# Performance work log

Hardware: AMD Instinct MI355X
Metric: run time of the kernel (lower is better)

Reference implementation:

```python
import jax, jax.numpy as jnp
import numpy as np
from jax import lax

B, IMG = 2, 512
FMC, HID, A, NC = 1024, 512, 9, 21
RED, POOL, TOP, IOU_THR = 16, 7, 20, 0.3
NEG = -1e30
# 3 scales x 3 aspect ratios (w, h)
ANCHOR_WH = np.array([[s * np.sqrt(r), s / np.sqrt(r)] for s in (64.0, 128.0, 256.0) for r in (0.5, 1.0, 2.0)], dtype=np.float32)


def conv(x, w, b, stride, pad):
    y = lax.conv_general_dilated(x, w, (stride, stride), pad, dimension_numbers=('NCHW', 'OIHW', 'NCHW'))
    return y + b[None, :, None, None]


def make_anchors(H, W, stride):
    cy = (jnp.arange(H, dtype=jnp.float32) + 0.5) * stride
    cx = (jnp.arange(W, dtype=jnp.float32) + 0.5) * stride
    cyg, cxg = jnp.meshgrid(cy, cx, indexing='ij')  # [H,W]
    wh = jnp.asarray(ANCHOR_WH)  # [A,2]
    w2 = wh[None, None, :, 0] / 2
    h2 = wh[None, None, :, 1] / 2
    cxg = cxg[:, :, None]
    cyg = cyg[:, :, None]
    boxes = jnp.stack([cxg - w2, cyg - h2, cxg + w2, cyg + h2], axis=-1)  # [H,W,A,4]
    return boxes.reshape(-1, 4)


def box_iou(b, boxes):
    # b [4], boxes [N,4], (x1,y1,x2,y2)
    ix1 = jnp.maximum(b[0], boxes[:, 0])
    iy1 = jnp.maximum(b[1], boxes[:, 1])
    ix2 = jnp.minimum(b[2], boxes[:, 2])
    iy2 = jnp.minimum(b[3], boxes[:, 3])
    inter = jnp.maximum(ix2 - ix1, 0.0) * jnp.maximum(iy2 - iy1, 0.0)
    ab = jnp.maximum(b[2] - b[0], 0.0) * jnp.maximum(b[3] - b[1], 0.0)
    ar = jnp.maximum(boxes[:, 2] - boxes[:, 0], 0.0) * jnp.maximum(boxes[:, 3] - boxes[:, 1], 0.0)
    return inter / (ab + ar - inter + 1e-8)


def nms_one(boxes, scores):
    # greedy NMS, fixed TOP selections
    n = scores.shape[0]
    idxs = jnp.arange(n)

    def step(s, _):
        i = jnp.argmax(s)
        b, sc = boxes[i], s[i]
        s = jnp.where((box_iou(b, boxes) > IOU_THR) | (idxs == i), NEG, s)
        return s, (b, sc)

    _, (bs, ss) = lax.scan(step, scores, None, length=TOP)
    return bs, ss  # [TOP,4], [TOP]


def roi_align_one(fm_b, boxes):
    # fm_b [C,H,W], boxes [R,4] in image coords -> [R,C,POOL,POOL]
    C, H, W = fm_b.shape
    b = boxes / RED
    t = (jnp.arange(POOL, dtype=jnp.float32) + 0.5) / POOL
    xs = b[:, 0:1] + jnp.maximum(b[:, 2] - b[:, 0], 0.0)[:, None] * t[None]  # [R,P]
    ys = b[:, 1:2] + jnp.maximum(b[:, 3] - b[:, 1], 0.0)[:, None] * t[None]
    x = jnp.clip(xs[:, None, :], 0.0, W - 1.0) * jnp.ones((1, POOL, 1), jnp.float32)  # [R,P,P]
    y = jnp.clip(ys[:, :, None], 0.0, H - 1.0) * jnp.ones((1, 1, POOL), jnp.float32)
    x0f, y0f = jnp.floor(x), jnp.floor(y)
    x0, y0 = x0f.astype(jnp.int32), y0f.astype(jnp.int32)
    x1 = jnp.minimum(x0 + 1, W - 1)
    y1 = jnp.minimum(y0 + 1, H - 1)
    lx, ly = x - x0f, y - y0f
    v00 = fm_b[:, y0, x0]
    v01 = fm_b[:, y0, x1]
    v10 = fm_b[:, y1, x0]
    v11 = fm_b[:, y1, x1]  # [C,R,P,P]
    out = v00 * (1 - ly) * (1 - lx) + v01 * (1 - ly) * lx + v10 * ly * (1 - lx) + v11 * ly * lx
    return out.transpose(1, 0, 2, 3)


def setup_inputs() -> dict:
    key = jax.random.key(0)
    ks = jax.random.split(key, 16)
    s = 0.02
    return {
        'img': jax.random.normal(ks[0], (B, 3, IMG, IMG), jnp.float32),
        'img_id': jnp.arange(B, dtype=jnp.int32),
        'cnn_w': jax.random.normal(ks[1], (FMC, 3, RED, RED), jnp.float32) * s,
        'cnn_b': jnp.zeros((FMC,), jnp.float32),
        'rpn_w': jax.random.normal(ks[2], (HID, FMC, 3, 3), jnp.float32) * s,
        'rpn_b': jnp.zeros((HID,), jnp.float32),
        'rpn_reg_w': jax.random.normal(ks[3], (A * 4, HID, 1, 1), jnp.float32) * s,
        'rpn_reg_b': jnp.zeros((A * 4,), jnp.float32),
        'rpn_cls_w': jax.random.normal(ks[4], (A, HID, 1, 1), jnp.float32) * s,
        'rpn_cls_b': jnp.zeros((A,), jnp.float32),
        'fc_w': jax.random.normal(ks[5], (FMC * POOL * POOL, 1024), jnp.float32) * 0.005,
        'fc_b': jnp.zeros((1024,), jnp.float32),
        'reg_w': jax.random.normal(ks[6], (1024, 4), jnp.float32) * s,
        'reg_b': jnp.zeros((4,), jnp.float32),
        'cls_w': jax.random.normal(ks[7], (1024, NC), jnp.float32) * s,
        'cls_b': jnp.zeros((NC,), jnp.float32),
    }


def reference(img, img_id, cnn_w, cnn_b, rpn_w, rpn_b, rpn_reg_w, rpn_reg_b, rpn_cls_w, rpn_cls_b, fc_w, fc_b, reg_w, reg_b, cls_w, cls_b):
    fm = jax.nn.relu(conv(img, cnn_w, cnn_b, RED, 'VALID'))  # [B,1024,32,32]
    Bn, C, H, W = fm.shape
    # sliding-window(3x3, stride 1) + per-slice RPN == 3x3 SAME conv + 1x1 heads
    h = jax.nn.relu(conv(fm, rpn_w, rpn_b, 1, 'SAME'))
    rpn_reg = conv(h, rpn_reg_w, rpn_reg_b, 1, 'SAME').transpose(0, 2, 3, 1).reshape(Bn, -1, 4)  # (h,w,a) order
    rpn_cls = conv(h, rpn_cls_w, rpn_cls_b, 1, 'SAME').transpose(0, 2, 3, 1).reshape(Bn, -1)
    anchors = make_anchors(H, W, RED)  # [H*W*A,4]
    nms_reg, nms_cls = jax.vmap(nms_one)(rpn_reg + anchors[None], rpn_cls)  # [B,TOP,4],[B,TOP]
    pooled = jax.vmap(roi_align_one)(fm[img_id], nms_reg)  # [B,TOP,C,P,P]
    flat = pooled.reshape(Bn * TOP, -1)
    hf = jax.nn.relu(flat @ fc_w + fc_b)
    rcnn_reg = (hf @ reg_w + reg_b).reshape(Bn, -1, 4)
    rcnn_cls = (hf @ cls_w + cls_b).reshape(Bn, TOP, -1)
    return rpn_reg, rpn_cls, nms_reg, nms_cls, rcnn_reg, rcnn_cls, anchors
```

## Files before the change

### kernel.cpp

```cpp
#include <hip/hip_runtime.h>
#include <math.h>


#define NEGV (-1e30f)

typedef unsigned short u16;
typedef float v4f __attribute__((ext_vector_type(4)));
typedef short short8 __attribute__((ext_vector_type(8)));

#define O_RPN_REG 0
#define O_RPN_CLS 73728
#define O_NMS_REG 92160
#define O_NMS_CLS 92320
#define O_RCNN_REG 92360
#define O_RCNN_CLS 92520
#define O_ANCH 93360

#define W_FM   0u
#define W_ZERO 2097152u
#define W_PROP 3145728u
#define W_SCR  3219456u
#define W_FLAT 3237888u
#define W_HF   5244928u
#define W_A1H  5285888u
#define W_A1L  6072320u
#define W_B1H  6858752u
#define W_B1L  7251968u
#define W_FMH  7645184u
#define W_FML  8693760u
#define W_B2H  9742336u
#define W_B2L  12101632u
#define W_PART 14460928u

static __device__ __forceinline__ float relu_(float v) { return fmaxf(v, 0.0f); }

static __device__ __forceinline__ void gload16(const void* g, void* l) {
    __builtin_amdgcn_global_load_lds(
        (const __attribute__((address_space(1))) unsigned int*)g,
        (__attribute__((address_space(3))) unsigned int*)l, 16, 0, 0);
}

static __device__ __forceinline__ u16 bf16_rtne(float x) {
    unsigned int u = __float_as_uint(x);
    unsigned int r = u + 0x7fffu + ((u >> 16) & 1u);
    return (u16)(r >> 16);
}
static __device__ __forceinline__ void split2(float x, u16& h, u16& l) {
    h = bf16_rtne(x);
    const float hf = __uint_as_float(((unsigned int)h) << 16);
    l = bf16_rtne(x - hf);
}
static __device__ __forceinline__ void split8_store(const float* v, u16* dsth, u16* dstl) {
    uint4 H, Lo;
    u16 h0, l0, h1, l1;
    split2(v[0], h0, l0); split2(v[1], h1, l1);
    H.x = (unsigned)h0 | ((unsigned)h1 << 16); Lo.x = (unsigned)l0 | ((unsigned)l1 << 16);
    split2(v[2], h0, l0); split2(v[3], h1, l1);
    H.y = (unsigned)h0 | ((unsigned)h1 << 16); Lo.y = (unsigned)l0 | ((unsigned)l1 << 16);
    split2(v[4], h0, l0); split2(v[5], h1, l1);
    H.z = (unsigned)h0 | ((unsigned)h1 << 16); Lo.z = (unsigned)l0 | ((unsigned)l1 << 16);
    split2(v[6], h0, l0); split2(v[7], h1, l1);
    H.w = (unsigned)h0 | ((unsigned)h1 << 16); Lo.w = (unsigned)l0 | ((unsigned)l1 << 16);
    *(uint4*)dsth = H; *(uint4*)dstl = Lo;
}

static __device__ __forceinline__ void anchor_wh(int a, float& w2, float& h2) {
    double s = (a < 3) ? 64.0 : (a < 6) ? 128.0 : 256.0;
    int rm = a - (a / 3) * 3;
    double r = (rm == 0) ? 0.5 : (rm == 1) ? 1.0 : 2.0;
    double sq = sqrt(r);
    w2 = (float)(s * sq) * 0.5f;
    h2 = (float)(s / sq) * 0.5f;
}

__global__ void k_prep_a1(const float* __restrict__ img, u16* __restrict__ a1h, u16* __restrict__ a1l,
                          float* __restrict__ zbuf) {
    if (blockIdx.x == 0 && threadIdx.x < 64) zbuf[threadIdx.x] = 0.0f;
    const int idx = blockIdx.x * 256 + threadIdx.x;
    const int m = idx / 192, kq = (idx - m * 192) * 4;
    const int b = m >> 10, i = (m >> 5) & 31, j = m & 31;
    const int c = kq >> 8, rem = kq & 255, y = rem >> 4, x = rem & 15;
    const float4 v = *(const float4*)(img + ((size_t)((b * 3 + c) * 512 + i * 16 + y)) * 512 + j * 16 + x);
    ushort4 H, Lo;
    split2(v.x, H.x, Lo.x); split2(v.y, H.y, Lo.y);
    split2(v.z, H.z, Lo.z); split2(v.w, H.w, Lo.w);
    *(ushort4*)(a1h + (size_t)idx * 4) = H;
    *(ushort4*)(a1l + (size_t)idx * 4) = Lo;
}

__global__ void k_split4(const float* __restrict__ src, u16* __restrict__ h, u16* __restrict__ l, int n4) {
    const int idx = blockIdx.x * 256 + threadIdx.x;
    if (idx >= n4) return;
    const float4 v = *(const float4*)(src + (size_t)idx * 4);
    ushort4 H, Lo;
    split2(v.x, H.x, Lo.x); split2(v.y, H.y, Lo.y);
    split2(v.z, H.z, Lo.z); split2(v.w, H.w, Lo.w);
    *(ushort4*)(h + (size_t)idx * 4) = H;
    *(ushort4*)(l + (size_t)idx * 4) = Lo;
}

__global__ __launch_bounds__(256) void k_prep_w2(const float* __restrict__ w,
        u16* __restrict__ bh, u16* __restrict__ bl) {
    __shared__ __align__(16) u16 sh[9216];
    __shared__ __align__(16) u16 sl[9216];
    const int oc = blockIdx.x;
    const float* p = w + (size_t)oc * 9216;
    for (int i = threadIdx.x * 4; i < 9216; i += 1024) {
        const float4 v = *(const float4*)(p + i);
        ushort4 H, Lo;
        split2(v.x, H.x, Lo.x); split2(v.y, H.y, Lo.y);
        split2(v.z, H.z, Lo.z); split2(v.w, H.w, Lo.w);
        *(ushort4*)(sh + i) = H;
        *(ushort4*)(sl + i) = Lo;
    }
    __syncthreads();
    const int ic4 = threadIdx.x * 4;
#pragma unroll
    for (int d = 0; d < 9; ++d) {
        ushort4 H, Lo;
        H.x = sh[(ic4 + 0) * 9 + d]; Lo.x = sl[(ic4 + 0) * 9 + d];
        H.y = sh[(ic4 + 1) * 9 + d]; Lo.y = sl[(ic4 + 1) * 9 + d];
        H.z = sh[(ic4 + 2) * 9 + d]; Lo.z = sl[(ic4 + 2) * 9 + d];
        H.w = sh[(ic4 + 3) * 9 + d]; Lo.w = sl[(ic4 + 3) * 9 + d];
        const size_t o = (size_t)oc * 9216 + d * 1024 + ic4;
        *(ushort4*)(bh + o) = H;
        *(ushort4*)(bl + o) = Lo;
    }
}

template<int MODE>
__global__ __launch_bounds__(256, 3) void k_gemm(
        const u16* __restrict__ Agh, const u16* __restrict__ Agl,
        const u16* __restrict__ Bgh, const u16* __restrict__ Bgl,
        const float* __restrict__ bias, float* __restrict__ Cout, float* __restrict__ Cout2,
        const int KA, const int KB, const int nchunk, const int ldc, const int do_bias_relu,
        u16* __restrict__ outH, u16* __restrict__ outL, const float* __restrict__ zbuf) {
    __shared__ __align__(16) u16 AsH[2 * 128 * 32];
    __shared__ __align__(16) u16 AsL[2 * 128 * 32];
    __shared__ __align__(16) u16 BsH[2 * 64 * 32];
    __shared__ __align__(16) u16 BsL[2 * 64 * 32];
    const int tid = threadIdx.x;
    const int w = tid >> 6, L = tid & 63;
    const int q = L >> 4, lr = L & 15;
    const int wm = w >> 1, wn = w & 1;
    const int m0 = blockIdx.x * 128, n0 = blockIdx.y * 64;
    const int zbase = blockIdx.z * nchunk;
    float* C;
    if (MODE == 1) {
        C = (blockIdx.z < 4) ? (Cout + (size_t)blockIdx.z * (2048u * 512u))
                             : (Cout2 + (size_t)(blockIdx.z - 4) * (2048u * 512u));
    } else {
        C = (blockIdx.z == 0) ? Cout : Cout2;
    }
    const int seg = L & 3, rsub = L >> 2;

    u16* lseg[6];
    int lsz[6];
    const u16* gbase[6];
    int arow_b[6], arow_i[6], arow_j[6];
    int kindv[6];
#pragma unroll
    for (int s = 0; s < 6; ++s) {
        const int idx = w * 6 + s;
        int kind, inst;
        if (idx < 8)       { kind = 0; inst = idx; }
        else if (idx < 16) { kind = 1; inst = idx - 8; }
        else if (idx < 20) { kind = 2; inst = idx - 16; }
        else               { kind = 3; inst = idx - 20; }
        kindv[s] = kind;
        const int r = inst * 16 + rsub;
        u16* lb = (kind == 0) ? AsH : (kind == 1) ? AsL : (kind == 2) ? BsH : BsL;
        lseg[s] = lb + r * 32 + seg * 8;
        lsz[s] = (kind < 2) ? (128 * 32) : (64 * 32);
        arow_b[s] = 0; arow_i[s] = 0; arow_j[s] = 0;
        if (kind >= 2) {
            const u16* gb = (kind == 2) ? Bgh : Bgl;
            gbase[s] = gb + (size_t)(n0 + r) * KB + seg * 8;
        } else if (MODE == 0) {
            const u16* gb = (kind == 0) ? Agh : Agl;
            gbase[s] = gb + (size_t)(m0 + r) * KA + seg * 8;
        } else {
            const int m = m0 + r;
            arow_b[s] = m >> 10; arow_i[s] = (m >> 5) & 31; arow_j[s] = m & 31;
            gbase[s] = (kind == 0) ? Agh : Agl;
        }
    }

    v4f acc[4][2];
#pragma unroll
    for (int t = 0; t < 4; ++t)
#pragma unroll
        for (int u2 = 0; u2 < 2; ++u2) acc[t][u2] = (v4f){0.f, 0.f, 0.f, 0.f};

#define ISSUE(c_, bb_) do { \
    int d_, ic_, kB_; \
    if (MODE == 0) { const int g_ = zbase + (c_); kB_ = g_ * 32; d_ = 0; ic_ = kB_; } \
    else { const int g_ = zbase + (c_); d_ = g_ >> 5; ic_ = (g_ & 31) << 5; kB_ = d_ * 1024 + ic_; } \
    const int di_ = d_ / 3, dj_ = d_ - di_ * 3; \
    _Pragma("unroll") \
    for (int s = 0; s < 6; ++s) { \
        const u16* gsrc_; \
        if (kindv[s] >= 2) gsrc_ = gbase[s] + kB_; \
        else if (MODE == 0) gsrc_ = gbase[s] + ic_; \
        else { \
            const int y_ = arow_i[s] + di_ - 1, x_ = arow_j[s] + dj_ - 1; \
            const bool ok_ = ((unsigned)y_ < 32u) && ((unsigned)x_ < 32u); \
            const int yc_ = ok_ ? y_ : 0, xc_ = ok_ ? x_ : 0; \
            const u16* ga_ = gbase[s] + (size_t)((arow_b[s] * 32 + yc_) * 32 + xc_) * 1024 + ic_ + seg * 8; \
            gsrc_ = ok_ ? ga_ : (const u16*)zbuf; \
        } \
        gload16(gsrc_, lseg[s] + (bb_) * lsz[s]); \
    } \
} while (0)

    int cur = 0;
    ISSUE(0, 0);
    for (int c = 0; c < nchunk; ++c) {
        __syncthreads();
        if (c + 1 < nchunk) ISSUE(c + 1, cur ^ 1);
        const int ao = cur * (128 * 32), bo = cur * (64 * 32);
        short8 ah[4], al[4], bh[2], bl[2];
#pragma unroll
        for (int t = 0; t < 4; ++t) {
            ah[t] = *(const short8*)(AsH + ao + (wm * 64 + t * 16 + lr) * 32 + q * 8);
            al[t] = *(const short8*)(AsL + ao + (wm * 64 + t * 16 + lr) * 32 + q * 8);
        }
#pragma unroll
        for (int u2 = 0; u2 < 2; ++u2) {
            bh[u2] = *(const short8*)(BsH + bo + (wn * 32 + u2 * 16 + lr) * 32 + q * 8);
            bl[u2] = *(const short8*)(BsL + bo + (wn * 32 + u2 * 16 + lr) * 32 + q * 8);
        }
#pragma unroll
        for (int t = 0; t < 4; ++t)
#pragma unroll
            for (int u2 = 0; u2 < 2; ++u2) {
                acc[t][u2] = __builtin_amdgcn_mfma_f32_16x16x32_bf16(ah[t], bh[u2], acc[t][u2], 0, 0, 0);
                acc[t][u2] = __builtin_amdgcn_mfma_f32_16x16x32_bf16(ah[t], bl[u2], acc[t][u2], 0, 0, 0);
                acc[t][u2] = __builtin_amdgcn_mfma_f32_16x16x32_bf16(al[t], bh[u2], acc[t][u2], 0, 0, 0);
            }
        cur ^= 1;
    }
#undef ISSUE

#pragma unroll
    for (int t = 0; t < 4; ++t) {
        const int row = m0 + wm * 64 + t * 16 + q * 4;
#pragma unroll
        for (int u2 = 0; u2 < 2; ++u2) {
            const int col = n0 + wn * 32 + u2 * 16 + lr;
            const float bv = do_bias_relu ? bias[col] : 0.f;
#pragma unroll
            for (int r = 0; r < 4; ++r) {
                float vv = acc[t][u2][r];
                if (do_bias_relu) vv = relu_(vv + bv);
                C[(size_t)(row + r) * ldc + col] = vv;
                if (MODE == 0 && outH != nullptr) {
                    u16 hh, ll; split2(vv, hh, ll);
                    outH[(size_t)(row + r) * 1024 + col] = hh;
                    outL[(size_t)(row + r) * 1024 + col] = ll;
                }
            }
        }
    }
}

__global__ void k_c1_reduce(const float* __restrict__ p1, const float* __restrict__ cb,
                            float* __restrict__ fm, u16* __restrict__ fmh, u16* __restrict__ fml) {
    const size_t o = ((size_t)blockIdx.x * 256 + threadIdx.x) * 4;
    float4 a = *(const float4*)(fm + o);
    const float4 b4 = *(const float4*)(p1 + o);
    const float4 bb = *(const float4*)(cb + (o & 1023));
    a.x = relu_(a.x + b4.x + bb.x);
    a.y = relu_(a.y + b4.y + bb.y);
    a.z = relu_(a.z + b4.z + bb.z);
    a.w = relu_(a.w + b4.w + bb.w);
    *(float4*)(fm + o) = a;
    ushort4 H, Lo;
    split2(a.x, H.x, Lo.x); split2(a.y, H.y, Lo.y);
    split2(a.z, H.z, Lo.z); split2(a.w, H.w, Lo.w);
    *(ushort4*)(fmh + o) = H;
    *(ushort4*)(fml + o) = Lo;
}

__global__ __launch_bounds__(64) void k_rpn_heads(const float* __restrict__ partA,
        const float* __restrict__ partB,
        const float* __restrict__ rpnb,
        const float* __restrict__ regw, const float* __restrict__ regb,
        const float* __restrict__ clsw, const float* __restrict__ clsb,
        float* __restrict__ out, float* __restrict__ prop, float* __restrict__ scr) {
    __shared__ __align__(16) float hrow[512];
    const int m = blockIdx.x, tid = threadIdx.x;
    const int b = m >> 10, qd = m & 1023, ii = qd >> 5, jj = qd & 31;
    for (int i = tid * 4; i < 512; i += 256) {
        const size_t ro = (size_t)m * 512 + i;
        const float4 a0 = *(const float4*)(partA + ro);
        const float4 a1 = *(const float4*)(partA + 1048576u + ro);
        const float4 a2 = *(const float4*)(partA + 2097152u + ro);
        const float4 a3 = *(const float4*)(partA + 3145728u + ro);
        const float4 a4 = *(const float4*)(partB + ro);
        const float4 a5 = *(const float4*)(partB + 1048576u + ro);
        const float4 bb = *(const float4*)(rpnb + i);
        float4 o;
        o.x = relu_(a0.x + a1.x + a2.x + a3.x + a4.x + a5.x + bb.x);
        o.y = relu_(a0.y + a1.y + a2.y + a3.y + a4.y + a5.y + bb.y);
        o.z = relu_(a0.z + a1.z + a2.z + a3.z + a4.z + a5.z + bb.z);
        o.w = relu_(a0.w + a1.w + a2.w + a3.w + a4.w + a5.w + bb.w);
        *(float4*)&hrow[i] = o;
    }
    __syncthreads();
    if (tid < 45) {
        const int isreg = (tid < 36);
        const float* wp = isreg ? (regw + (size_t)tid * 512) : (clsw + (size_t)(tid - 36) * 512);
        float acc2 = isreg ? regb[tid] : clsb[tid - 36];
        for (int k = 0; k < 512; k += 4) {
            const float4 wv = *(const float4*)(wp + k);
            acc2 += hrow[k + 0] * wv.x; acc2 += hrow[k + 1] * wv.y;
            acc2 += hrow[k + 2] * wv.z; acc2 += hrow[k + 3] * wv.w;
        }
        if (isreg) {
            out[O_RPN_REG + (size_t)b * 36864 + qd * 36 + tid] = acc2;
            const int a = tid >> 2, cc = tid & 3;
            float w2, h2; anchor_wh(a, w2, h2);
            const float cx = ((float)jj + 0.5f) * 16.f, cy = ((float)ii + 0.5f) * 16.f;
            const float av = (cc == 0) ? cx - w2 : (cc == 1) ? cy - h2 : (cc == 2) ? cx + w2 : cy + h2;
            prop[(size_t)b * 36864 + qd * 36 + tid] = acc2 + av;
        } else {
            const int n = tid - 36;
            out[O_RPN_CLS + (size_t)b * 9216 + qd * 9 + n] = acc2;
            scr[(size_t)b * 9216 + qd * 9 + n] = acc2;
        }
    }
    if (b == 0 && tid >= 48 && tid < 57) {
        const int a = tid - 48;
        float w2, h2; anchor_wh(a, w2, h2);
        const float cx = ((float)jj + 0.5f) * 16.f, cy = ((float)ii + 0.5f) * 16.f;
        const float4 av4 = make_float4(cx - w2, cy - h2, cx + w2, cy + h2);
        *(float4*)(out + O_ANCH + (size_t)(qd * 9 + a) * 4) = av4;
    }
}

__global__ __launch_bounds__(512) void k_nms3(const float* __restrict__ prop,
        const float* __restrict__ scr, float* __restrict__ out) {
    __shared__ float wv_[2][8];
    __shared__ int wi_[2][8];
    const int b = blockIdx.x, tid = threadIdx.x;
    const int lane = tid & 63, wid = tid >> 6;
    const float* P = prop + (size_t)b * 36864;
    float4 bx[18]; float sv[18];
#pragma unroll
    for (int k = 0; k < 18; ++k) {
        const int i = tid * 18 + k;
        bx[k] = *(const float4*)(P + (size_t)i * 4);
        sv[k] = scr[b * 9216 + i];
    }
    for (int t = 0; t < 20; ++t) {
        float bv = -3.4e38f; int bi = 0;
#pragma unroll
        for (int k = 0; k < 18; ++k)
            if (sv[k] > bv) { bv = sv[k]; bi = tid * 18 + k; }
#pragma unroll
        for (int off = 1; off < 64; off <<= 1) {
            const float ov = __shfl_xor(bv, off);
            const int oi = __shfl_xor(bi, off);
            if (ov > bv || (ov == bv && oi < bi)) { bv = ov; bi = oi; }
        }
        if (lane == 0) { wv_[t & 1][wid] = bv; wi_[t & 1][wid] = bi; }
        __syncthreads();
        float rb = wv_[t & 1][0]; int sel = wi_[t & 1][0];
#pragma unroll
        for (int j = 1; j < 8; ++j) {
            const float v2 = wv_[t & 1][j]; const int i2 = wi_[t & 1][j];
            if (v2 > rb || (v2 == rb && i2 < sel)) { rb = v2; sel = i2; }
        }
        const float4 bb = *(const float4*)(P + (size_t)sel * 4);
        if (tid == 0) {
            *(float4*)(out + O_NMS_REG + (size_t)(b * 20 + t) * 4) = bb;
            out[O_NMS_CLS + b * 20 + t] = rb;
        }
        const float ab2 = fmaxf(bb.z - bb.x, 0.f) * fmaxf(bb.w - bb.y, 0.f);
#pragma unroll
        for (int k = 0; k < 18; ++k) {
            const float ix1 = fmaxf(bb.x, bx[k].x), iy1 = fmaxf(bb.y, bx[k].y);
            const float ix2 = fminf(bb.z, bx[k].z), iy2 = fminf(bb.w, bx[k].w);
            const float inter = fmaxf(ix2 - ix1, 0.f) * fmaxf(iy2 - iy1, 0.f);
            const float ar2 = fmaxf(bx[k].z - bx[k].x, 0.f) * fmaxf(bx[k].w - bx[k].y, 0.f);
            const float iou = inter / (ab2 + ar2 - inter + 1e-8f);
            if (iou > 0.3f || (tid * 18 + k) == sel) sv[k] = NEGV;
        }
    }
}

__global__ __launch_bounds__(256) void k_roi(const float* __restrict__ fm,
        const int* __restrict__ img_id, const float* __restrict__ nreg,
        float* __restrict__ flat) {
    __shared__ float tile[12544];
    const int c0 = blockIdx.x * 256;
    const int roi = blockIdx.y, b = blockIdx.z;
    const float* bx = nreg + (size_t)(b * 20 + roi) * 4;
    const float b0 = bx[0] * 0.0625f, b1 = bx[1] * 0.0625f;
    const float b2 = bx[2] * 0.0625f, b3 = bx[3] * 0.0625f;
    const float wd = fmaxf(b2 - b0, 0.f), hg = fmaxf(b3 - b1, 0.f);
    const int bb = img_id[b];
    const float* fmb = fm + (size_t)bb * (32 * 32 * 1024);
    const int c = c0 + threadIdx.x;
    for (int py = 0; py < 7; ++py) {
        const float tyv = ((float)py + 0.5f) / 7.0f;
        const float ycv = fminf(fmaxf(b1 + hg * tyv, 0.f), 31.f);
        const float y0f = floorf(ycv);
        const int y0 = (int)y0f, y1 = min(y0 + 1, 31);
        const float ly = ycv - y0f, omly = 1.f - ly;
        for (int px = 0; px < 7; ++px) {
            const float txv = ((float)px + 0.5f) / 7.0f;
            const float xcv = fminf(fmaxf(b0 + wd * txv, 0.f), 31.f);
            const float x0f = floorf(xcv);
            const int x0 = (int)x0f, x1 = min(x0 + 1, 31);
            const float lx = xcv - x0f, omlx = 1.f - lx;
            const int o00 = ((y0 * 32) + x0) << 10, o01 = ((y0 * 32) + x1) << 10;
            const int o10 = ((y1 * 32) + x0) << 10, o11 = ((y1 * 32) + x1) << 10;
            const float v00 = fmb[o00 + c], v01 = fmb[o01 + c];
            const float v10 = fmb[o10 + c], v11 = fmb[o11 + c];
            tile[threadIdx.x * 49 + py * 7 + px] =
                ((v00 * omly) * omlx) + ((v01 * omly) * lx)
                + ((v10 * ly) * omlx) + ((v11 * ly) * lx);
        }
    }
    __syncthreads();
    const size_t ob = (size_t)(b * 20 + roi) * 50176 + (size_t)c0 * 49;
    for (int i = threadIdx.x * 4; i < 12544; i += 1024)
        *(float4*)(flat + ob + i) = *(const float4*)&tile[i];
}

__global__ void k_hf_init(const float* __restrict__ fcb, float* __restrict__ hf) {
    const int i = blockIdx.x * 256 + threadIdx.x;
    if (i < 40 * 1024) hf[i] = fcb[i & 1023];
}

__global__ __launch_bounds__(256, 2) void k_fc_mfma(const float* __restrict__ flat,
        const float* __restrict__ fcw, float* __restrict__ hf) {
    __shared__ __align__(16) u16 AsH[4 * 48 * 8];
    __shared__ __align__(16) u16 AsL[4 * 48 * 8];
    __shared__ __align__(16) u16 BsH[4 * 256 * 8];
    __shared__ __align__(16) u16 BsL[4 * 256 * 8];
    const int tid = threadIdx.x;
    const int w = tid >> 6, L = tid & 63, q = L >> 4, lr = L & 15;
    const int n0 = blockIdx.x * 256, kb = blockIdx.y * 512;
    if (tid < 32) {
        const int oct = tid >> 3, m = 40 + (tid & 7);
        *(uint4*)(AsH + (oct * 48 + m) * 8) = make_uint4(0, 0, 0, 0);
        *(uint4*)(AsL + (oct * 48 + m) * 8) = make_uint4(0, 0, 0, 0);
    }
    const int am = tid >> 2, aoct = tid & 3;
    const float* abase = flat + (size_t)am * 50176 + kb + aoct * 8;
    const float* bcol = fcw + n0 + tid;

    v4f acc[3][4];
#pragma unroll
    for (int mt = 0; mt < 3; ++mt)
#pragma unroll
        for (int nt = 0; nt < 4; ++nt) acc[mt][nt] = (v4f){0.f, 0.f, 0.f, 0.f};

    float areg[8];
    float breg[4][8];

#define LOADF(c_) do { \
    if (tid < 160) { \
        const float4 u_ = *(const float4*)(abase + (c_) * 32); \
        const float4 v_ = *(const float4*)(abase + (c_) * 32 + 4); \
        areg[0] = u_.x; areg[1] = u_.y; areg[2] = u_.z; areg[3] = u_.w; \
        areg[4] = v_.x; areg[5] = v_.y; areg[6] = v_.z; areg[7] = v_.w; \
    } \
    _Pragma("unroll") \
    for (int o_ = 0; o_ < 4; ++o_) \
        _Pragma("unroll") \
        for (int j_ = 0; j_ < 8; ++j_) \
            breg[o_][j_] = bcol[(size_t)(kb + (c_) * 32 + o_ * 8 + j_) * 1024]; \
} while (0)

    LOADF(0);
    for (int c = 0; c < 16; ++c) {
        __syncthreads();
        if (tid < 160)
            split8_store(areg, AsH + (aoct * 48 + am) * 8, AsL + (aoct * 48 + am) * 8);
#pragma unroll
        for (int o = 0; o < 4; ++o)
            split8_store(breg[o], BsH + (o * 256 + tid) * 8, BsL + (o * 256 + tid) * 8);
        __syncthreads();
        if (c + 1 < 16) LOADF(c + 1);
        short8 ah[3], al[3], bh2[4], bl2[4];
#pragma unroll
        for (int mt = 0; mt < 3; ++mt) {
            ah[mt] = *(const short8*)(AsH + (q * 48 + mt * 16 + lr) * 8);
            al[mt] = *(const short8*)(AsL + (q * 48 + mt * 16 + lr) * 8);
        }
#pragma unroll
        for (int nt = 0; nt < 4; ++nt) {
            bh2[nt] = *(const short8*)(BsH + (q * 256 + w * 64 + nt * 16 + lr) * 8);
            bl2[nt] = *(const short8*)(BsL + (q * 256 + w * 64 + nt * 16 + lr) * 8);
        }
#pragma unroll
        for (int mt = 0; mt < 3; ++mt)
#pragma unroll
            for (int nt = 0; nt < 4; ++nt) {
                acc[mt][nt] = __builtin_amdgcn_mfma_f32_16x16x32_bf16(ah[mt], bh2[nt], acc[mt][nt], 0, 0, 0);
                acc[mt][nt] = __builtin_amdgcn_mfma_f32_16x16x32_bf16(ah[mt], bl2[nt], acc[mt][nt], 0, 0, 0);
                acc[mt][nt] = __builtin_amdgcn_mfma_f32_16x16x32_bf16(al[mt], bh2[nt], acc[mt][nt], 0, 0, 0);
            }
    }
#undef LOADF

#pragma unroll
    for (int mt = 0; mt < 3; ++mt) {
#pragma unroll
        for (int nt = 0; nt < 4; ++nt) {
#pragma unroll
            for (int r = 0; r < 4; ++r) {
                const int row = mt * 16 + q * 4 + r;
                if (row < 40)
                    atomicAdd(hf + (size_t)row * 1024 + n0 + w * 64 + nt * 16 + lr, acc[mt][nt][r]);
            }
        }
    }
}

__global__ __launch_bounds__(64) void k_heads(const float* __restrict__ hf,
        const float* __restrict__ regw, const float* __restrict__ regb,
        const float* __restrict__ clsw, const float* __restrict__ clsb,
        float* __restrict__ out) {
    __shared__ __align__(16) float hrow[1024];
    const int m = blockIdx.x, tid = threadIdx.x;
    for (int i = tid * 4; i < 1024; i += 256) {
        const float4 v = *(const float4*)(hf + (size_t)m * 1024 + i);
        hrow[i + 0] = relu_(v.x); hrow[i + 1] = relu_(v.y);
        hrow[i + 2] = relu_(v.z); hrow[i + 3] = relu_(v.w);
    }
    __syncthreads();
    if (tid < 25) {
        float acc2 = 0.f;
        if (tid < 4) {
            for (int k = 0; k < 1024; ++k) acc2 += hrow[k] * regw[(size_t)k * 4 + tid];
            out[O_RCNN_REG + m * 4 + tid] = acc2 + regb[tid];
        } else {
            const int n = tid - 4;
            for (int k = 0; k < 1024; ++k) acc2 += hrow[k] * clsw[(size_t)k * 21 + n];
            out[O_RCNN_CLS + m * 21 + n] = acc2 + clsb[n];
        }
    }
}

extern "C" void kernel_launch(void* const* d_in, const int* in_sizes, int n_in,
                              void* d_out, int out_size, void* d_ws, size_t ws_size,
                              hipStream_t stream) {
    (void)in_sizes; (void)n_in; (void)out_size; (void)ws_size;
    const float* img       = (const float*)d_in[0];
    const int*   img_id    = (const int*)  d_in[1];
    const float* cnn_w     = (const float*)d_in[2];
    const float* cnn_b     = (const float*)d_in[3];
    const float* rpn_w     = (const float*)d_in[4];
    const float* rpn_b     = (const float*)d_in[5];
    const float* rpn_reg_w = (const float*)d_in[6];
    const float* rpn_reg_b = (const float*)d_in[7];
    const float* rpn_cls_w = (const float*)d_in[8];
    const float* rpn_cls_b = (const float*)d_in[9];
    const float* fc_w      = (const float*)d_in[10];
    const float* fc_b      = (const float*)d_in[11];
    const float* reg_w     = (const float*)d_in[12];
    const float* reg_b     = (const float*)d_in[13];
    const float* cls_w     = (const float*)d_in[14];
    const float* cls_b     = (const float*)d_in[15];
    float* out = (float*)d_out;
    float* ws  = (float*)d_ws;

    float* fm   = ws + W_FM;
    float* zbuf = ws + W_ZERO;
    float* prop = ws + W_PROP;
    float* scr  = ws + W_SCR;
    float* flat = ws + W_FLAT;
    float* hf   = ws + W_HF;
    u16* a1h = (u16*)(ws + W_A1H);
    u16* a1l = (u16*)(ws + W_A1L);
    u16* b1h = (u16*)(ws + W_B1H);
    u16* b1l = (u16*)(ws + W_B1L);
    u16* fmh = (u16*)(ws + W_FMH);
    u16* fml = (u16*)(ws + W_FML);
    u16* b2h = (u16*)(ws + W_B2H);
    u16* b2l = (u16*)(ws + W_B2L);
    float* partA = ws + W_FLAT;
    float* partB = ws + W_PART;

    k_prep_a1<<<1536, 256, 0, stream>>>(img, a1h, a1l, zbuf);
    k_split4<<<768, 256, 0, stream>>>(cnn_w, b1h, b1l, 196608);
    k_prep_w2<<<512, 256, 0, stream>>>(rpn_w, b2h, b2l);
    k_gemm<0><<<dim3(16, 16, 2), 256, 0, stream>>>(a1h, a1l, b1h, b1l, cnn_b, fm, partB,
                                                   768, 768, 12, 1024, 0, nullptr, nullptr, zbuf);
    k_c1_reduce<<<2048, 256, 0, stream>>>(partB, cnn_b, fm, fmh, fml);
    k_gemm<1><<<dim3(16, 8, 6), 256, 0, stream>>>(fmh, fml, b2h, b2l, nullptr, partA, partB,
                                                  1024, 9216, 48, 512, 0, nullptr, nullptr, zbuf);
    k_rpn_heads<<<2048, 64, 0, stream>>>(partA, partB, rpn_b, rpn_reg_w, rpn_reg_b, rpn_cls_w, rpn_cls_b,
                                         out, prop, scr);
    k_nms3<<<2, 512, 0, stream>>>(prop, scr, out);
    k_roi<<<dim3(4, 20, 2), 256, 0, stream>>>(fm, img_id, out + O_NMS_REG, flat);
    k_hf_init<<<160, 256, 0, stream>>>(fc_b, hf);
    k_fc_mfma<<<dim3(4, 98), 256, 0, stream>>>(flat, fc_w, hf);
    k_heads<<<40, 64, 0, stream>>>(hf, reg_w, reg_b, cls_w, cls_b, out);
}
```

Measured before the change: 593.2 us.

## Merge prep kernels, batch RPN head rows, fold hf init, narrow FC tiles

New measurement: 605.4 us. 2.1% more time.

```diff
diff --git a/kernel.cpp b/kernel.cpp
--- a/kernel.cpp
+++ b/kernel.cpp
@@ -73,58 +73,58 @@
     h2 = (float)(s / sq) * 0.5f;
 }
 
-__global__ void k_prep_a1(const float* __restrict__ img, u16* __restrict__ a1h, u16* __restrict__ a1l,
-                          float* __restrict__ zbuf) {
-    if (blockIdx.x == 0 && threadIdx.x < 64) zbuf[threadIdx.x] = 0.0f;
-    const int idx = blockIdx.x * 256 + threadIdx.x;
-    const int m = idx / 192, kq = (idx - m * 192) * 4;
-    const int b = m >> 10, i = (m >> 5) & 31, j = m & 31;
-    const int c = kq >> 8, rem = kq & 255, y = rem >> 4, x = rem & 15;
-    const float4 v = *(const float4*)(img + ((size_t)((b * 3 + c) * 512 + i * 16 + y)) * 512 + j * 16 + x);
-    ushort4 H, Lo;
-    split2(v.x, H.x, Lo.x); split2(v.y, H.y, Lo.y);
-    split2(v.z, H.z, Lo.z); split2(v.w, H.w, Lo.w);
-    *(ushort4*)(a1h + (size_t)idx * 4) = H;
-    *(ushort4*)(a1l + (size_t)idx * 4) = Lo;
-}
-
-__global__ void k_split4(const float* __restrict__ src, u16* __restrict__ h, u16* __restrict__ l, int n4) {
-    const int idx = blockIdx.x * 256 + threadIdx.x;
-    if (idx >= n4) return;
-    const float4 v = *(const float4*)(src + (size_t)idx * 4);
-    ushort4 H, Lo;
-    split2(v.x, H.x, Lo.x); split2(v.y, H.y, Lo.y);
-    split2(v.z, H.z, Lo.z); split2(v.w, H.w, Lo.w);
-    *(ushort4*)(h + (size_t)idx * 4) = H;
-    *(ushort4*)(l + (size_t)idx * 4) = Lo;
-}
-
-__global__ __launch_bounds__(256) void k_prep_w2(const float* __restrict__ w,
-        u16* __restrict__ bh, u16* __restrict__ bl) {
+__global__ __launch_bounds__(256) void k_prep_all(
+        const float* __restrict__ img, u16* __restrict__ a1h, u16* __restrict__ a1l,
+        float* __restrict__ zbuf,
+        const float* __restrict__ cnnw, u16* __restrict__ b1h, u16* __restrict__ b1l,
+        const float* __restrict__ rpnw, u16* __restrict__ b2h, u16* __restrict__ b2l) {
     __shared__ __align__(16) u16 sh[9216];
     __shared__ __align__(16) u16 sl[9216];
-    const int oc = blockIdx.x;
-    const float* p = w + (size_t)oc * 9216;
-    for (int i = threadIdx.x * 4; i < 9216; i += 1024) {
-        const float4 v = *(const float4*)(p + i);
+    const int bx = blockIdx.x, tid = threadIdx.x;
+    if (bx < 1536) {
+        if (bx == 0 && tid < 64) zbuf[tid] = 0.0f;
+        const int idx = bx * 256 + tid;
+        const int m = idx / 192, kq = (idx - m * 192) * 4;
+        const int b = m >> 10, i = (m >> 5) & 31, j = m & 31;
+        const int c = kq >> 8, rem = kq & 255, y = rem >> 4, x = rem & 15;
+        const float4 v = *(const float4*)(img + ((size_t)((b * 3 + c) * 512 + i * 16 + y)) * 512 + j * 16 + x);
         ushort4 H, Lo;
         split2(v.x, H.x, Lo.x); split2(v.y, H.y, Lo.y);
         split2(v.z, H.z, Lo.z); split2(v.w, H.w, Lo.w);
-        *(ushort4*)(sh + i) = H;
-        *(ushort4*)(sl + i) = Lo;
-    }
-    __syncthreads();
-    const int ic4 = threadIdx.x * 4;
-#pragma unroll
-    for (int d = 0; d < 9; ++d) {
+        *(ushort4*)(a1h + (size_t)idx * 4) = H;
+        *(ushort4*)(a1l + (size_t)idx * 4) = Lo;
+    } else if (bx < 2304) {
+        const int idx = (bx - 1536) * 256 + tid;
+        const float4 v = *(const float4*)(cnnw + (size_t)idx * 4);
         ushort4 H, Lo;
-        H.x = sh[(ic4 + 0) * 9 + d]; Lo.x = sl[(ic4 + 0) * 9 + d];
-        H.y = sh[(ic4 + 1) * 9 + d]; Lo.y = sl[(ic4 + 1) * 9 + d];
-        H.z = sh[(ic4 + 2) * 9 + d]; Lo.z = sl[(ic4 + 2) * 9 + d];
-        H.w = sh[(ic4 + 3) * 9 + d]; Lo.w = sl[(ic4 + 3) * 9 + d];
-        const size_t o = (size_t)oc * 9216 + d * 1024 + ic4;
-        *(ushort4*)(bh + o) = H;
-        *(ushort4*)(bl + o) = Lo;
+        split2(v.x, H.x, Lo.x); split2(v.y, H.y, Lo.y);
+        split2(v.z, H.z, Lo.z); split2(v.w, H.w, Lo.w);
+        *(ushort4*)(b1h + (size_t)idx * 4) = H;
+        *(ushort4*)(b1l + (size_t)idx * 4) = Lo;
+    } else {
+        const int oc = bx - 2304;
+        const float* p = rpnw + (size_t)oc * 9216;
+        for (int i = tid * 4; i < 9216; i += 1024) {
+            const float4 v = *(const float4*)(p + i);
+            ushort4 H, Lo;
+            split2(v.x, H.x, Lo.x); split2(v.y, H.y, Lo.y);
+            split2(v.z, H.z, Lo.z); split2(v.w, H.w, Lo.w);
+            *(ushort4*)(sh + i) = H;
+            *(ushort4*)(sl + i) = Lo;
+        }
+        __syncthreads();
+        const int ic4 = tid * 4;
+#pragma unroll
+        for (int d = 0; d < 9; ++d) {
+            ushort4 H, Lo;
+            H.x = sh[(ic4 + 0) * 9 + d]; Lo.x = sl[(ic4 + 0) * 9 + d];
+            H.y = sh[(ic4 + 1) * 9 + d]; Lo.y = sl[(ic4 + 1) * 9 + d];
+            H.z = sh[(ic4 + 2) * 9 + d]; Lo.z = sl[(ic4 + 2) * 9 + d];
+            H.w = sh[(ic4 + 3) * 9 + d]; Lo.w = sl[(ic4 + 3) * 9 + d];
+            const size_t o = (size_t)oc * 9216 + d * 1024 + ic4;
+            *(ushort4*)(b2h + o) = H;
+            *(ushort4*)(b2l + o) = Lo;
+        }
     }
 }
 
@@ -282,60 +282,69 @@
     *(ushort4*)(fml + o) = Lo;
 }
 
-__global__ __launch_bounds__(64) void k_rpn_heads(const float* __restrict__ partA,
+__global__ __launch_bounds__(256) void k_rpn_heads2(const float* __restrict__ partA,
         const float* __restrict__ partB,
         const float* __restrict__ rpnb,
         const float* __restrict__ regw, const float* __restrict__ regb,
         const float* __restrict__ clsw, const float* __restrict__ clsb,
         float* __restrict__ out, float* __restrict__ prop, float* __restrict__ scr) {
-    __shared__ __align__(16) float hrow[512];
-    const int m = blockIdx.x, tid = threadIdx.x;
-    const int b = m >> 10, qd = m & 1023, ii = qd >> 5, jj = qd & 31;
-    for (int i = tid * 4; i < 512; i += 256) {
-        const size_t ro = (size_t)m * 512 + i;
+    __shared__ __align__(16) float hrow[8][512];
+    const int tid = threadIdx.x;
+    const int m0 = blockIdx.x * 8;
+#pragma unroll
+    for (int i = 0; i < 4; ++i) {
+        const int f = i * 256 + tid;
+        const int r = f >> 7, c4 = (f & 127) * 4;
+        const size_t ro = (size_t)(m0 + r) * 512 + c4;
         const float4 a0 = *(const float4*)(partA + ro);
         const float4 a1 = *(const float4*)(partA + 1048576u + ro);
         const float4 a2 = *(const float4*)(partA + 2097152u + ro);
         const float4 a3 = *(const float4*)(partA + 3145728u + ro);
         const float4 a4 = *(const float4*)(partB + ro);
         const float4 a5 = *(const float4*)(partB + 1048576u + ro);
-        const float4 bb = *(const float4*)(rpnb + i);
+        const float4 bb = *(const float4*)(rpnb + c4);
         float4 o;
         o.x = relu_(a0.x + a1.x + a2.x + a3.x + a4.x + a5.x + bb.x);
         o.y = relu_(a0.y + a1.y + a2.y + a3.y + a4.y + a5.y + bb.y);
         o.z = relu_(a0.z + a1.z + a2.z + a3.z + a4.z + a5.z + bb.z);
         o.w = relu_(a0.w + a1.w + a2.w + a3.w + a4.w + a5.w + bb.w);
-        *(float4*)&hrow[i] = o;
+        *(float4*)&hrow[r][c4] = o;
     }
     __syncthreads();
-    if (tid < 45) {
-        const int isreg = (tid < 36);
-        const float* wp = isreg ? (regw + (size_t)tid * 512) : (clsw + (size_t)(tid - 36) * 512);
-        float acc2 = isreg ? regb[tid] : clsb[tid - 36];
-        for (int k = 0; k < 512; k += 4) {
-            const float4 wv = *(const float4*)(wp + k);
-            acc2 += hrow[k + 0] * wv.x; acc2 += hrow[k + 1] * wv.y;
-            acc2 += hrow[k + 2] * wv.z; acc2 += hrow[k + 3] * wv.w;
-        }
-        if (isreg) {
-            out[O_RPN_REG + (size_t)b * 36864 + qd * 36 + tid] = acc2;
-            const int a = tid >> 2, cc = tid & 3;
+    const int w = tid >> 6, lane = tid & 63;
+#pragma unroll
+    for (int rr = 0; rr < 2; ++rr) {
+        const int lrow = w * 2 + rr;
+        const int m = m0 + lrow;
+        const int b = m >> 10, qd = m & 1023, ii = qd >> 5, jj = qd & 31;
+        const float cx = ((float)jj + 0.5f) * 16.f, cy = ((float)ii + 0.5f) * 16.f;
+        if (lane < 45) {
+            const int isreg = (lane < 36);
+            const float* wp = isreg ? (regw + (size_t)lane * 512) : (clsw + (size_t)(lane - 36) * 512);
+            float acc2 = isreg ? regb[lane] : clsb[lane - 36];
+            const float* hr = hrow[lrow];
+            for (int k = 0; k < 512; k += 4) {
+                const float4 wv = *(const float4*)(wp + k);
+                acc2 += hr[k + 0] * wv.x; acc2 += hr[k + 1] * wv.y;
+                acc2 += hr[k + 2] * wv.z; acc2 += hr[k + 3] * wv.w;
+            }
+            if (isreg) {
+                out[O_RPN_REG + (size_t)b * 36864 + qd * 36 + lane] = acc2;
+                const int a = lane >> 2, cc = lane & 3;
+                float w2, h2; anchor_wh(a, w2, h2);
+                const float av = (cc == 0) ? cx - w2 : (cc == 1) ? cy - h2 : (cc == 2) ? cx + w2 : cy + h2;
+                prop[(size_t)b * 36864 + qd * 36 + lane] = acc2 + av;
+            } else {
+                const int n = lane - 36;
+                out[O_RPN_CLS + (size_t)b * 9216 + qd * 9 + n] = acc2;
+                scr[(size_t)b * 9216 + qd * 9 + n] = acc2;
+            }
+        } else if (b == 0 && lane < 54) {
+            const int a = lane - 45;
             float w2, h2; anchor_wh(a, w2, h2);
-            const float cx = ((float)jj + 0.5f) * 16.f, cy = ((float)ii + 0.5f) * 16.f;
-            const float av = (cc == 0) ? cx - w2 : (cc == 1) ? cy - h2 : (cc == 2) ? cx + w2 : cy + h2;
-            prop[(size_t)b * 36864 + qd * 36 + tid] = acc2 + av;
-        } else {
-            const int n = tid - 36;
-            out[O_RPN_CLS + (size_t)b * 9216 + qd * 9 + n] = acc2;
-            scr[(size_t)b * 9216 + qd * 9 + n] = acc2;
-        }
-    }
-    if (b == 0 && tid >= 48 && tid < 57) {
-        const int a = tid - 48;
-        float w2, h2; anchor_wh(a, w2, h2);
-        const float cx = ((float)jj + 0.5f) * 16.f, cy = ((float)ii + 0.5f) * 16.f;
-        const float4 av4 = make_float4(cx - w2, cy - h2, cx + w2, cy + h2);
-        *(float4*)(out + O_ANCH + (size_t)(qd * 9 + a) * 4) = av4;
+            const float4 av4 = make_float4(cx - w2, cy - h2, cx + w2, cy + h2);
+            *(float4*)(out + O_ANCH + (size_t)(qd * 9 + a) * 4) = av4;
+        }
     }
 }
 
@@ -392,8 +401,10 @@
 
 __global__ __launch_bounds__(256) void k_roi(const float* __restrict__ fm,
         const int* __restrict__ img_id, const float* __restrict__ nreg,
-        float* __restrict__ flat) {
+        float* __restrict__ flat, const float* __restrict__ fcb, float* __restrict__ hf) {
     __shared__ float tile[12544];
+    const int hid = (((blockIdx.z * 20 + blockIdx.y) * 4) + blockIdx.x) * 256 + threadIdx.x;
+    hf[hid] = fcb[hid & 1023];
     const int c0 = blockIdx.x * 256;
     const int roi = blockIdx.y, b = blockIdx.z;
     const float* bx = nreg + (size_t)(b * 20 + roi) * 4;
@@ -430,20 +441,15 @@
         *(float4*)(flat + ob + i) = *(const float4*)&tile[i];
 }
 
-__global__ void k_hf_init(const float* __restrict__ fcb, float* __restrict__ hf) {
-    const int i = blockIdx.x * 256 + threadIdx.x;
-    if (i < 40 * 1024) hf[i] = fcb[i & 1023];
-}
-
 __global__ __launch_bounds__(256, 2) void k_fc_mfma(const float* __restrict__ flat,
         const float* __restrict__ fcw, float* __restrict__ hf) {
     __shared__ __align__(16) u16 AsH[4 * 48 * 8];
     __shared__ __align__(16) u16 AsL[4 * 48 * 8];
-    __shared__ __align__(16) u16 BsH[4 * 256 * 8];
-    __shared__ __align__(16) u16 BsL[4 * 256 * 8];
+    __shared__ __align__(16) u16 BsH[4 * 128 * 8];
+    __shared__ __align__(16) u16 BsL[4 * 128 * 8];
     const int tid = threadIdx.x;
     const int w = tid >> 6, L = tid & 63, q = L >> 4, lr = L & 15;
-    const int n0 = blockIdx.x * 256, kb = blockIdx.y * 512;
+    const int n0 = blockIdx.x * 128, kb = blockIdx.y * 512;
     if (tid < 32) {
         const int oct = tid >> 3, m = 40 + (tid & 7);
         *(uint4*)(AsH + (oct * 48 + m) * 8) = make_uint4(0, 0, 0, 0);
@@ -451,16 +457,17 @@
     }
     const int am = tid >> 2, aoct = tid & 3;
     const float* abase = flat + (size_t)am * 50176 + kb + aoct * 8;
-    const float* bcol = fcw + n0 + tid;
-
-    v4f acc[3][4];
+    const int bcolI = tid & 127, bkh = tid >> 7;
+    const float* bcol = fcw + n0 + bcolI;
+
+    v4f acc[3][2];
 #pragma unroll
     for (int mt = 0; mt < 3; ++mt)
 #pragma unroll
-        for (int nt = 0; nt < 4; ++nt) acc[mt][nt] = (v4f){0.f, 0.f, 0.f, 0.f};
+        for (int nt = 0; nt < 2; ++nt) acc[mt][nt] = (v4f){0.f, 0.f, 0.f, 0.f};
 
     float areg[8];
-    float breg[4][8];
+    float breg[2][8];
 
 #define LOADF(c_) do { \
     if (tid < 160) { \
@@ -470,10 +477,10 @@
         areg[4] = v_.x; areg[5] = v_.y; areg[6] = v_.z; areg[7] = v_.w; \
     } \
     _Pragma("unroll") \
-    for (int o_ = 0; o_ < 4; ++o_) \
+    for (int o_ = 0; o_ < 2; ++o_) \
         _Pragma("unroll") \
         for (int j_ = 0; j_ < 8; ++j_) \
-            breg[o_][j_] = bcol[(size_t)(kb + (c_) * 32 + o_ * 8 + j_) * 1024]; \
+            breg[o_][j_] = bcol[(size_t)(kb + (c_) * 32 + bkh * 16 + o_ * 8 + j_) * 1024]; \
 } while (0)
 
     LOADF(0);
@@ -482,25 +489,26 @@
         if (tid < 160)
             split8_store(areg, AsH + (aoct * 48 + am) * 8, AsL + (aoct * 48 + am) * 8);
 #pragma unroll
-        for (int o = 0; o < 4; ++o)
-            split8_store(breg[o], BsH + (o * 256 + tid) * 8, BsL + (o * 256 + tid) * 8);
+        for (int o = 0; o < 2; ++o)
+            split8_store(breg[o], BsH + ((bkh * 2 + o) * 128 + bcolI) * 8,
+                                  BsL + ((bkh * 2 + o) * 128 + bcolI) * 8);
         __syncthreads();
         if (c + 1 < 16) LOADF(c + 1);
-        short8 ah[3], al[3], bh2[4], bl2[4];
+        short8 ah[3], al[3], bh2[2], bl2[2];
 #pragma unroll
         for (int mt = 0; mt < 3; ++mt) {
             ah[mt] = *(const short8*)(AsH + (q * 48 + mt * 16 + lr) * 8);
             al[mt] = *(const short8*)(AsL + (q * 48 + mt * 16 + lr) * 8);
         }
 #pragma unroll
-        for (int nt = 0; nt < 4; ++nt) {
-            bh2[nt] = *(const short8*)(BsH + (q * 256 + w * 64 + nt * 16 + lr) * 8);
-            bl2[nt] = *(const short8*)(BsL + (q * 256 + w * 64 + nt * 16 + lr) * 8);
+        for (int nt = 0; nt < 2; ++nt) {
+            bh2[nt] = *(const short8*)(BsH + (q * 128 + w * 32 + nt * 16 + lr) * 8);
+            bl2[nt] = *(const short8*)(BsL + (q * 128 + w * 32 + nt * 16 + lr) * 8);
         }
 #pragma unroll
         for (int mt = 0; mt < 3; ++mt)
 #pragma unroll
-            for (int nt = 0; nt < 4; ++nt) {
+            for (int nt = 0; nt < 2; ++nt) {
                 acc[mt][nt] = __builtin_amdgcn_mfma_f32_16x16x32_bf16(ah[mt], bh2[nt], acc[mt][nt], 0, 0, 0);
                 acc[mt][nt] = __builtin_amdgcn_mfma_f32_16x16x32_bf16(ah[mt], bl2[nt], acc[mt][nt], 0, 0, 0);
                 acc[mt][nt] = __builtin_amdgcn_mfma_f32_16x16x32_bf16(al[mt], bh2[nt], acc[mt][nt], 0, 0, 0);
@@ -511,12 +519,12 @@
 #pragma unroll
     for (int mt = 0; mt < 3; ++mt) {
 #pragma unroll
-        for (int nt = 0; nt < 4; ++nt) {
+        for (int nt = 0; nt < 2; ++nt) {
 #pragma unroll
             for (int r = 0; r < 4; ++r) {
                 const int row = mt * 16 + q * 4 + r;
                 if (row < 40)
-                    atomicAdd(hf + (size_t)row * 1024 + n0 + w * 64 + nt * 16 + lr, acc[mt][nt][r]);
+                    atomicAdd(hf + (size_t)row * 1024 + n0 + w * 32 + nt * 16 + lr, acc[mt][nt][r]);
             }
         }
     }
@@ -587,19 +595,16 @@
     float* partA = ws + W_FLAT;
     float* partB = ws + W_PART;
 
-    k_prep_a1<<<1536, 256, 0, stream>>>(img, a1h, a1l, zbuf);
-    k_split4<<<768, 256, 0, stream>>>(cnn_w, b1h, b1l, 196608);
-    k_prep_w2<<<512, 256, 0, stream>>>(rpn_w, b2h, b2l);
+    k_prep_all<<<2816, 256, 0, stream>>>(img, a1h, a1l, zbuf, cnn_w, b1h, b1l, rpn_w, b2h, b2l);
     k_gemm<0><<<dim3(16, 16, 2), 256, 0, stream>>>(a1h, a1l, b1h, b1l, cnn_b, fm, partB,
                                                    768, 768, 12, 1024, 0, nullptr, nullptr, zbuf);
     k_c1_reduce<<<2048, 256, 0, stream>>>(partB, cnn_b, fm, fmh, fml);
     k_gemm<1><<<dim3(16, 8, 6), 256, 0, stream>>>(fmh, fml, b2h, b2l, nullptr, partA, partB,
                                                   1024, 9216, 48, 512, 0, nullptr, nullptr, zbuf);
-    k_rpn_heads<<<2048, 64, 0, stream>>>(partA, partB, rpn_b, rpn_reg_w, rpn_reg_b, rpn_cls_w, rpn_cls_b,
-                                         out, prop, scr);
+    k_rpn_heads2<<<256, 256, 0, stream>>>(partA, partB, rpn_b, rpn_reg_w, rpn_reg_b, rpn_cls_w, rpn_cls_b,
+                                          out, prop, scr);
     k_nms3<<<2, 512, 0, stream>>>(prop, scr, out);
-    k_roi<<<dim3(4, 20, 2), 256, 0, stream>>>(fm, img_id, out + O_NMS_REG, flat);
-    k_hf_init<<<160, 256, 0, stream>>>(fc_b, hf);
-    k_fc_mfma<<<dim3(4, 98), 256, 0, stream>>>(flat, fc_w, hf);
+    k_roi<<<dim3(4, 20, 2), 256, 0, stream>>>(fm, img_id, out + O_NMS_REG, flat, fc_b, hf);
+    k_fc_mfma<<<dim3(8, 98), 256, 0, stream>>>(flat, fc_w, hf);
     k_heads<<<40, 64, 0, stream>>>(hf, reg_w, reg_b, cls_w, cls_b, out);
 }
```
